# Performance work log

Measured on AMD Instinct MI355X. Metric: run time of the kernel, lower is better.

The kernel has to match this reference:

```python
import jax, jax.numpy as jnp
import numpy as np

N_VARS = 50000
N_EDGES = 400000
HIDDEN = 128


def setup_inputs() -> dict:
    key = jax.random.key(0)
    k1, k2, k3 = jax.random.split(key, 3)
    x = jax.random.normal(k1, (N_VARS, HIDDEN), dtype=jnp.float32)
    # torch Linear(2H, H, bias=False): weight shape [H, 2H]
    W = jax.random.normal(k2, (HIDDEN, 2 * HIDDEN), dtype=jnp.float32) * (1.0 / np.sqrt(2 * HIDDEN))
    edge_idx = jax.random.randint(k3, (2, N_EDGES), 0, N_VARS, dtype=jnp.int32)
    return {"x": x, "W": W, "edge_idx": edge_idx}


def reference(x, W, edge_idx):
    # Symmetrize edges: append reversed edges -> [2, 2E]
    src = jnp.concatenate([edge_idx[0], edge_idx[1]])  # [2E]
    dst = jnp.concatenate([edge_idx[1], edge_idx[0]])  # [2E]
    # Gather endpoint features and concat -> [2E, 2H]
    m = jnp.concatenate([x[src], x[dst]], axis=1)
    # Small dense linear (no bias): [2E, 2H] @ [2H, H] -> [2E, H]
    m = m @ W.T
    # scatter_sum over destination index, dim_size = num_vars
    r = jax.ops.segment_sum(m, dst, num_segments=x.shape[0])
    return r
```

## Files before the change

kernel.cpp:

```cpp
#include <hip/hip_runtime.h>

#define N_VARS   50000
#define N_EDGES  400000
#define HID      128
#define MTILES   (N_VARS / 16)
#define MPB      4
#define GEMM_BLOCKS ((MTILES + MPB - 1) / MPB)
#define NBKT     196
#define NDST_PAD (NBKT * 256)
#define CAP      64
#define CAP2     48
#define ABLOCKS  391

#define Y1_B0   0
#define Y1_SZ   (N_VARS * HID)
#define Y2_B0   (Y1_B0 + Y1_SZ)
#define Y2_SZ   (N_VARS * HID * 2)
#define SRC_B0  (Y2_B0 + Y2_SZ)
#define SRC_SZ  (NDST_PAD * CAP * 2)
#define BLK_B0  (SRC_B0 + SRC_SZ)
#define BLK_SZ  (ABLOCKS * NBKT * 4)
#define CUR_B0  (BLK_B0 + BLK_SZ)
#define CUR_SZ  (NDST_PAD * 4)
#define CO_B0   (CUR_B0 + CUR_SZ)

typedef __attribute__((ext_vector_type(8))) short bf16x8;
typedef __attribute__((ext_vector_type(4))) float f32x4;
typedef __attribute__((ext_vector_type(2))) float f32x2;

__device__ __forceinline__ unsigned short f2bf(float f) {
    unsigned u = __builtin_bit_cast(unsigned, f);
    unsigned r = u + 0x7fffu + ((u >> 16) & 1u);
    return (unsigned short)(r >> 16);
}

__device__ __forceinline__ bf16x8 cvt8(float4 a0, float4 a1) {
    bf16x8 r;
    r[0] = (short)f2bf(a0.x); r[1] = (short)f2bf(a0.y);
    r[2] = (short)f2bf(a0.z); r[3] = (short)f2bf(a0.w);
    r[4] = (short)f2bf(a1.x); r[5] = (short)f2bf(a1.y);
    r[6] = (short)f2bf(a1.z); r[7] = (short)f2bf(a1.w);
    return r;
}

__global__ __launch_bounds__(256) void gemm_binA_kernel(
    const float* __restrict__ x, const float* __restrict__ W,
    const int* __restrict__ e,
    unsigned char* __restrict__ y1f8, unsigned short* __restrict__ y2b,
    int* __restrict__ blkcnt, int* __restrict__ coarse2) {
    __shared__ int cnt[NBKT];
    const int t = threadIdx.x;

    if (blockIdx.x < GEMM_BLOCKS) {
        const int lane = t & 63;
        const int wv   = t >> 6;
        const int ml   = lane & 15;
        const int quad = lane >> 4;

        bf16x8 bfrag[4][4];
#pragma unroll
        for (int i = 0; i < 4; ++i) {
            const int n = (wv * 4 + i) * 16 + ml;
            const float* wrow = (n < HID) ? (W + (size_t)n * 256)
                                          : (W + (size_t)(n - HID) * 256 + HID);
#pragma unroll
            for (int kc = 0; kc < 4; ++kc) {
                const float4* w4 = (const float4*)(wrow + kc * 32 + quad * 8);
                bfrag[i][kc] = cvt8(w4[0], w4[1]);
            }
        }

#pragma unroll
        for (int mi = 0; mi < MPB; ++mi) {
            const int mt = blockIdx.x * MPB + mi;
            if (mt >= MTILES) break;
            const int v = mt * 16 + ml;

            bf16x8 afrag[4];
#pragma unroll
            for (int kc = 0; kc < 4; ++kc) {
                const float4* ap = (const float4*)(x + (size_t)v * HID + kc * 32 + quad * 8);
                afrag[kc] = cvt8(ap[0], ap[1]);
            }

            f32x4 acc[4];
#pragma unroll
            for (int i = 0; i < 4; ++i) acc[i] = f32x4{0.f, 0.f, 0.f, 0.f};
#pragma unroll
            for (int kc = 0; kc < 4; ++kc)
#pragma unroll
                for (int i = 0; i < 4; ++i)
                    acc[i] = __builtin_amdgcn_mfma_f32_16x16x32_bf16(bfrag[i][kc], afrag[kc], acc[i], 0, 0, 0);

            if (wv < 2) {
#pragma unroll
                for (int i = 0; i < 4; ++i) {
                    int w = __builtin_amdgcn_cvt_pk_fp8_f32(acc[i][0], acc[i][1], 0, false);
                    w     = __builtin_amdgcn_cvt_pk_fp8_f32(acc[i][2], acc[i][3], w, true);
                    *(int*)(y1f8 + (size_t)v * HID + wv * 64 + i * 16 + quad * 4) = w;
                }
            } else {
#pragma unroll
                for (int i = 0; i < 4; ++i) {
                    uint2 p;
                    p.x = (unsigned)f2bf(acc[i][0]) | ((unsigned)f2bf(acc[i][1]) << 16);
                    p.y = (unsigned)f2bf(acc[i][2]) | ((unsigned)f2bf(acc[i][3]) << 16);
                    *(uint2*)(y2b + (size_t)v * HID + (wv - 2) * 64 + i * 16 + quad * 4) = p;
                }
            }
        }
    } else {
        const int bA = blockIdx.x - GEMM_BLOCKS;
        for (int i = t; i < NBKT; i += 256) cnt[i] = 0;
        __syncthreads();

        int e0[4], e1[4], nb = 0;
        const int b0 = (bA * 256 + t) * 4;
        if (bA < ABLOCKS - 1) {
            int4 A = *(const int4*)(e + b0);
            int4 B = *(const int4*)(e + N_EDGES + b0);
            e0[0] = A.x; e0[1] = A.y; e0[2] = A.z; e0[3] = A.w;
            e1[0] = B.x; e1[1] = B.y; e1[2] = B.z; e1[3] = B.w;
            nb = 4;
        } else {
            for (int j = 0; j < 4; ++j)
                if (b0 + j < N_EDGES) { e0[nb] = e[b0 + j]; e1[nb] = e[N_EDGES + b0 + j]; ++nb; }
        }

        int* myregion = coarse2 + (size_t)bA * NBKT * CAP2;
#pragma unroll 4
        for (int j = 0; j < nb; ++j) {
            int a = e0[j], b = e1[j];
            int bk0 = b >> 8, bk1 = a >> 8;
            int p0  = (a << 8) | (b & 255);
            int p1  = (b << 8) | (a & 255);
            int l0  = atomicAdd(&cnt[bk0], 1);
            if (l0 < CAP2) myregion[bk0 * CAP2 + l0] = p0;
            int l1  = atomicAdd(&cnt[bk1], 1);
            if (l1 < CAP2) myregion[bk1 * CAP2 + l1] = p1;
        }
        __syncthreads();
        for (int i = t; i < NBKT; i += 256) {
            int c = cnt[i];
            blkcnt[bA * NBKT + i] = (c < CAP2) ? c : CAP2;
        }
    }
}

__global__ __launch_bounds__(256) void binB_kernel(const int* __restrict__ blkcnt,
                                                   const int* __restrict__ coarse2,
                                                   unsigned short* __restrict__ srcs,
                                                   int* __restrict__ cursor) {
    __shared__ int fcnt[256];
    __shared__ unsigned short fine[256 * CAP];
    const int t = threadIdx.x, b = blockIdx.x;
    fcnt[t] = 0;
    __syncthreads();

    for (int s = t; s < ABLOCKS; s += 256) {
        int c = blkcnt[s * NBKT + b];
        const int* seg = coarse2 + (size_t)(s * NBKT + b) * CAP2;
        for (int i = 0; i < c; ++i) {
            int p = seg[i];
            int dl = p & 255;
            int pos = atomicAdd(&fcnt[dl], 1);
            if (pos < CAP) fine[dl * CAP + pos] = (unsigned short)(p >> 8);
        }
    }
    __syncthreads();

    const uint4* fs = (const uint4*)fine;
    uint4* gs = (uint4*)(srcs + (size_t)b * 256 * CAP);
#pragma unroll
    for (int k = 0; k < 8; ++k) gs[k * 256 + t] = fs[k * 256 + t];
    cursor[b * 256 + t] = fcnt[t];
}

__global__ __launch_bounds__(256) void gather_kernel(const unsigned char* __restrict__ y1f8,
                                                     const unsigned short* __restrict__ y2b,
                                                     const int* __restrict__ cursor,
                                                     const unsigned short* __restrict__ srcs,
                                                     float* __restrict__ out) {
    const int t    = threadIdx.x;
    const int v    = blockIdx.x * 32 + (t >> 3);
    const int lane = t & 7;
    if (v >= N_VARS) return;
    const int c = cursor[v];
    const int n = (c < CAP) ? c : CAP;
    const unsigned short* bucket = srcs + (size_t)v * CAP;

    const uint4* base = (const uint4*)y1f8;
    float acc[16];
#pragma unroll
    for (int i = 0; i < 16; ++i) acc[i] = 0.f;

    auto accum = [&](uint4 a) {
        int u[4] = {(int)a.x, (int)a.y, (int)a.z, (int)a.w};
#pragma unroll
        for (int w = 0; w < 4; ++w) {
            f32x2 lo = __builtin_amdgcn_cvt_pk_f32_fp8(u[w], false);
            f32x2 hi = __builtin_amdgcn_cvt_pk_f32_fp8(u[w], true);
            acc[4 * w + 0] += lo[0];
            acc[4 * w + 1] += lo[1];
            acc[4 * w + 2] += hi[0];
            acc[4 * w + 3] += hi[1];
        }
    };

    int j = 0;
    for (; j + 4 <= n; j += 4) {
        int s0 = bucket[j + 0], s1 = bucket[j + 1];
        int s2 = bucket[j + 2], s3 = bucket[j + 3];
        uint4 a0 = base[(size_t)s0 * 8 + lane];
        uint4 a1 = base[(size_t)s1 * 8 + lane];
        uint4 a2 = base[(size_t)s2 * 8 + lane];
        uint4 a3 = base[(size_t)s3 * 8 + lane];
        accum(a0); accum(a1); accum(a2); accum(a3);
    }
    for (; j < n; ++j) accum(base[(size_t)bucket[j] * 8 + lane]);

    const uint4* y2p = (const uint4*)(y2b + (size_t)v * HID) + lane * 2;
    uint4 w0 = y2p[0], w1 = y2p[1];
    unsigned uu[8] = {w0.x, w0.y, w0.z, w0.w, w1.x, w1.y, w1.z, w1.w};
    const float dg = (float)c;
    float4* op = (float4*)(out + (size_t)v * HID + lane * 16);
#pragma unroll
    for (int q = 0; q < 4; ++q) {
        float b0 = __builtin_bit_cast(float, uu[2 * q] << 16);
        float b1 = __builtin_bit_cast(float, uu[2 * q] & 0xffff0000u);
        float b2 = __builtin_bit_cast(float, uu[2 * q + 1] << 16);
        float b3 = __builtin_bit_cast(float, uu[2 * q + 1] & 0xffff0000u);
        float4 o = {dg * b0 + acc[4 * q + 0], dg * b1 + acc[4 * q + 1],
                    dg * b2 + acc[4 * q + 2], dg * b3 + acc[4 * q + 3]};
        op[q] = o;
    }
}

extern "C" void kernel_launch(void* const* d_in, const int* in_sizes, int n_in,
                              void* d_out, int out_size, void* d_ws, size_t ws_size,
                              hipStream_t stream) {
    const float* x = (const float*)d_in[0];
    const float* W = (const float*)d_in[1];
    const int*   e = (const int*)d_in[2];
    float* out = (float*)d_out;

    unsigned char* wsb = (unsigned char*)d_ws;
    unsigned char*  y1f8   = wsb + Y1_B0;
    unsigned short* y2b    = (unsigned short*)(wsb + Y2_B0);
    unsigned short* srcs   = (unsigned short*)(wsb + SRC_B0);
    int*            blkcnt = (int*)(wsb + BLK_B0);
    int*            cursor = (int*)(wsb + CUR_B0);
    int*            coarse2 = (int*)(wsb + CO_B0);

    gemm_binA_kernel<<<GEMM_BLOCKS + ABLOCKS, 256, 0, stream>>>(
        x, W, e, y1f8, y2b, blkcnt, coarse2);
    binB_kernel<<<NBKT, 256, 0, stream>>>(blkcnt, coarse2, srcs, cursor);
    gather_kernel<<<(N_VARS + 31) / 32, 256, 0, stream>>>(y1f8, y2b, cursor, srcs, out);
}
```

Before: 142.0 us.

## Compact coarse binning with global atomic offsets and precompute W bf16 fragments

```diff
diff --git a/kernel.cpp b/kernel.cpp
--- a/kernel.cpp
+++ b/kernel.cpp
@@ -4,25 +4,26 @@
 #define N_EDGES  400000
 #define HID      128
 #define MTILES   (N_VARS / 16)
-#define MPB      4
-#define GEMM_BLOCKS ((MTILES + MPB - 1) / MPB)
+#define GEMM_BLOCKS ((MTILES + 1) / 2)
 #define NBKT     196
+#define CCAP     4608
 #define NDST_PAD (NBKT * 256)
 #define CAP      64
-#define CAP2     48
 #define ABLOCKS  391
 
 #define Y1_B0   0
 #define Y1_SZ   (N_VARS * HID)
 #define Y2_B0   (Y1_B0 + Y1_SZ)
 #define Y2_SZ   (N_VARS * HID * 2)
-#define SRC_B0  (Y2_B0 + Y2_SZ)
+#define WB_B0   (Y2_B0 + Y2_SZ)
+#define WB_SZ   (64 * 64 * 8 * 2)
+#define SRC_B0  (WB_B0 + WB_SZ)
 #define SRC_SZ  (NDST_PAD * CAP * 2)
-#define BLK_B0  (SRC_B0 + SRC_SZ)
-#define BLK_SZ  (ABLOCKS * NBKT * 4)
-#define CUR_B0  (BLK_B0 + BLK_SZ)
-#define CUR_SZ  (NDST_PAD * 4)
-#define CO_B0   (CUR_B0 + CUR_SZ)
+#define INT_B0  (SRC_B0 + SRC_SZ)
+
+#define I_GCOUNT 0
+#define I_CURSOR (I_GCOUNT + NBKT)
+#define I_COARSE (I_CURSOR + NDST_PAD)
 
 typedef __attribute__((ext_vector_type(8))) short bf16x8;
 typedef __attribute__((ext_vector_type(4))) float f32x4;
@@ -43,12 +44,31 @@
     return r;
 }
 
+__global__ __launch_bounds__(256) void prep_kernel(const float* __restrict__ W,
+                                                   short* __restrict__ wb,
+                                                   int* __restrict__ gcount) {
+    int gid = blockIdx.x * 256 + threadIdx.x;
+    if (gid < NBKT) gcount[gid] = 0;
+    if (gid < 4096) {
+        int f = gid >> 6, lane = gid & 63;
+        int nt = f >> 2, kc = f & 3;
+        int ml = lane & 15, quad = lane >> 4;
+        int n = nt * 16 + ml;
+        const float* wp = (n < HID) ? (W + (size_t)n * 256)
+                                    : (W + (size_t)(n - HID) * 256 + HID);
+        wp += kc * 32 + quad * 8;
+        const float4* w4 = (const float4*)wp;
+        *(bf16x8*)(wb + (size_t)f * 512 + lane * 8) = cvt8(w4[0], w4[1]);
+    }
+}
+
 __global__ __launch_bounds__(256) void gemm_binA_kernel(
-    const float* __restrict__ x, const float* __restrict__ W,
+    const float* __restrict__ x, const short* __restrict__ wb,
     const int* __restrict__ e,
     unsigned char* __restrict__ y1f8, unsigned short* __restrict__ y2b,
-    int* __restrict__ blkcnt, int* __restrict__ coarse2) {
+    int* __restrict__ gcount, int* __restrict__ coarse) {
     __shared__ int cnt[NBKT];
+    __shared__ int base[NBKT];
     const int t = threadIdx.x;
 
     if (blockIdx.x < GEMM_BLOCKS) {
@@ -59,20 +79,14 @@
 
         bf16x8 bfrag[4][4];
 #pragma unroll
-        for (int i = 0; i < 4; ++i) {
-            const int n = (wv * 4 + i) * 16 + ml;
-            const float* wrow = (n < HID) ? (W + (size_t)n * 256)
-                                          : (W + (size_t)(n - HID) * 256 + HID);
-#pragma unroll
-            for (int kc = 0; kc < 4; ++kc) {
-                const float4* w4 = (const float4*)(wrow + kc * 32 + quad * 8);
-                bfrag[i][kc] = cvt8(w4[0], w4[1]);
-            }
-        }
-
-#pragma unroll
-        for (int mi = 0; mi < MPB; ++mi) {
-            const int mt = blockIdx.x * MPB + mi;
+        for (int i = 0; i < 4; ++i)
+#pragma unroll
+            for (int kc = 0; kc < 4; ++kc)
+                bfrag[i][kc] = *(const bf16x8*)(wb + (size_t)((wv * 4 + i) * 4 + kc) * 512 + lane * 8);
+
+#pragma unroll
+        for (int mi = 0; mi < 2; ++mi) {
+            const int mt = blockIdx.x * 2 + mi;
             if (mt >= MTILES) break;
             const int v = mt * 16 + ml;
 
@@ -127,28 +141,31 @@
                 if (b0 + j < N_EDGES) { e0[nb] = e[b0 + j]; e1[nb] = e[N_EDGES + b0 + j]; ++nb; }
         }
 
-        int* myregion = coarse2 + (size_t)bA * NBKT * CAP2;
+        int bkt[8], lpos[8], pk[8];
 #pragma unroll 4
         for (int j = 0; j < nb; ++j) {
             int a = e0[j], b = e1[j];
-            int bk0 = b >> 8, bk1 = a >> 8;
-            int p0  = (a << 8) | (b & 255);
-            int p1  = (b << 8) | (a & 255);
-            int l0  = atomicAdd(&cnt[bk0], 1);
-            if (l0 < CAP2) myregion[bk0 * CAP2 + l0] = p0;
-            int l1  = atomicAdd(&cnt[bk1], 1);
-            if (l1 < CAP2) myregion[bk1 * CAP2 + l1] = p1;
+            bkt[2 * j]      = b >> 8;
+            pk[2 * j]       = (a << 8) | (b & 255);
+            lpos[2 * j]     = atomicAdd(&cnt[b >> 8], 1);
+            bkt[2 * j + 1]  = a >> 8;
+            pk[2 * j + 1]   = (b << 8) | (a & 255);
+            lpos[2 * j + 1] = atomicAdd(&cnt[a >> 8], 1);
         }
         __syncthreads();
-        for (int i = t; i < NBKT; i += 256) {
-            int c = cnt[i];
-            blkcnt[bA * NBKT + i] = (c < CAP2) ? c : CAP2;
-        }
-    }
-}
-
-__global__ __launch_bounds__(256) void binB_kernel(const int* __restrict__ blkcnt,
-                                                   const int* __restrict__ coarse2,
+        for (int i = t; i < NBKT; i += 256)
+            base[i] = (cnt[i] > 0) ? atomicAdd(&gcount[i], cnt[i]) : 0;
+        __syncthreads();
+
+        for (int j = 0; j < 2 * nb; ++j) {
+            int p = base[bkt[j]] + lpos[j];
+            if (p < CCAP) coarse[bkt[j] * CCAP + p] = pk[j];
+        }
+    }
+}
+
+__global__ __launch_bounds__(256) void binB_kernel(const int* __restrict__ gcount,
+                                                   const int* __restrict__ coarse,
                                                    unsigned short* __restrict__ srcs,
                                                    int* __restrict__ cursor) {
     __shared__ int fcnt[256];
@@ -157,15 +174,19 @@
     fcnt[t] = 0;
     __syncthreads();
 
-    for (int s = t; s < ABLOCKS; s += 256) {
-        int c = blkcnt[s * NBKT + b];
-        const int* seg = coarse2 + (size_t)(s * NBKT + b) * CAP2;
-        for (int i = 0; i < c; ++i) {
-            int p = seg[i];
-            int dl = p & 255;
-            int pos = atomicAdd(&fcnt[dl], 1);
-            if (pos < CAP) fine[dl * CAP + pos] = (unsigned short)(p >> 8);
-        }
+    int n = gcount[b];
+    if (n > CCAP) n = CCAP;
+    const int* cb = coarse + b * CCAP;
+
+    int i = t;
+    int p = (i < n) ? cb[i] : 0;
+    while (i < n) {
+        int pn = (i + 256 < n) ? cb[i + 256] : 0;
+        int dl = p & 255;
+        int pos = atomicAdd(&fcnt[dl], 1);
+        if (pos < CAP) fine[dl * CAP + pos] = (unsigned short)(p >> 8);
+        p = pn;
+        i += 256;
     }
     __syncthreads();
 
@@ -247,13 +268,16 @@
     unsigned char* wsb = (unsigned char*)d_ws;
     unsigned char*  y1f8   = wsb + Y1_B0;
     unsigned short* y2b    = (unsigned short*)(wsb + Y2_B0);
+    short*          wb     = (short*)(wsb + WB_B0);
     unsigned short* srcs   = (unsigned short*)(wsb + SRC_B0);
-    int*            blkcnt = (int*)(wsb + BLK_B0);
-    int*            cursor = (int*)(wsb + CUR_B0);
-    int*            coarse2 = (int*)(wsb + CO_B0);
-
+    int*            wsi    = (int*)(wsb + INT_B0);
+    int*            gcount = wsi + I_GCOUNT;
+    int*            cursor = wsi + I_CURSOR;
+    int*            coarse = wsi + I_COARSE;
+
+    prep_kernel<<<17, 256, 0, stream>>>(W, wb, gcount);
     gemm_binA_kernel<<<GEMM_BLOCKS + ABLOCKS, 256, 0, stream>>>(
-        x, W, e, y1f8, y2b, blkcnt, coarse2);
-    binB_kernel<<<NBKT, 256, 0, stream>>>(blkcnt, coarse2, srcs, cursor);
+        x, wb, e, y1f8, y2b, gcount, coarse);
+    binB_kernel<<<NBKT, 256, 0, stream>>>(gcount, coarse, srcs, cursor);
     gather_kernel<<<(N_VARS + 31) / 32, 256, 0, stream>>>(y1f8, y2b, cursor, srcs, out);
 }
```

Result: faster. 132.4 us (-6.8%).
